# Performance work log

Measured on AMD Instinct MI355X. Metric: run time of the kernel, lower is better.

## Reference

```python
import jax, jax.numpy as jnp
import numpy as np

CUTOFF = 5.0       # module __init__ arg
BOX_L = 40.0       # side of cubic region positions are drawn from (OBC: no box passed)
N_ATOMS = 8192
MAX_PAIRS = 1_048_576  # static bound on directed pairs (expected ~550k)


def setup_inputs() -> dict:
    key = jax.random.key(0)
    positions = jax.random.uniform(key, (N_ATOMS, 3), dtype=jnp.float32) * BOX_L
    return {"positions": positions}


def _pairwise_dist(x):
    # Euclidean distance matrix via the gram trick (avoids [N,N,3] intermediate).
    sq = jnp.sum(x * x, axis=1)
    d2 = sq[:, None] + sq[None, :] - 2.0 * (x @ x.T)
    return jnp.sqrt(jnp.maximum(d2, 0.0))


def _safe_norm(dr):
    # norm with zero-safe gradient (padded pairs have dr == 0)
    d2 = jnp.sum(dr * dr, axis=1)
    ok = d2 > 0
    return jnp.where(ok, jnp.sqrt(jnp.where(ok, d2, 1.0)), 0.0)


def reference(positions):
    n = positions.shape[0]
    dist = _pairwise_dist(positions)                      # [N, N]
    mask = (dist < CUTOFF) & (~jnp.eye(n, dtype=bool))    # exclude self-pairs
    # torch.argwhere equivalent, padded to static size; padding -> (0, 0)
    i, j = jnp.nonzero(mask, size=MAX_PAIRS, fill_value=0)
    pairs = jnp.stack([i, j], axis=1).astype(jnp.int32)   # [MAX_PAIRS, 2]
    # pairs_buffer_scales: 1 where i < j else 0 (padding (0,0) -> 0)
    buffer_scales = (i < j).astype(jnp.int32)
    # pairs_ds (pbc_flag=False): ||r_j - r_i||
    dr = positions[j] - positions[i]                      # [MAX_PAIRS, 3]
    ds = _safe_norm(dr)
    return pairs, buffer_scales, ds
```

## Files before the change

### kernel.cpp

```cpp
#include <hip/hip_runtime.h>

#define MAXP 1048576
#define NATOMS 8192
#define D2_CUT 0x1.8ffffep+4f
#define CINV 0.175f
#define CAP 192

#define W_SORTPOS 0
#define W_SORTID  32768
#define W_ROWCNT  36864
#define W_GRPSUM  45056
#define W_CELLOFF 45568
#define W_JBUF    46080

__device__ __forceinline__ float sq3_nc(float x, float y, float z) {
#pragma clang fp contract(off)
  float a = x * x;
  float b = y * y;
  float c = z * z;
  return (a + b) + c;
}

__device__ __forceinline__ float d2_gram(float xi, float yi, float zi, float sqi,
                                         float xj, float yj, float zj, float sqj) {
#pragma clang fp contract(off)
  float g = xi * xj;
  g = __builtin_fmaf(yi, yj, g);
  g = __builtin_fmaf(zi, zj, g);
  float t = sqi + sqj;
  float d2 = t - 2.0f * g;
  return d2;
}

__device__ __forceinline__ float d2_direct(float xi, float yi, float zi,
                                           float xj, float yj, float zj) {
#pragma clang fp contract(off)
  float dx = xj - xi;
  float dy = yj - yi;
  float dz = zj - zi;
  float a = dx * dx;
  float b = dy * dy;
  float c = dz * dz;
  return (a + b) + c;
}

__device__ __forceinline__ int cellco(float v) {
  int c = (int)(v * CINV);
  return c < 0 ? 0 : (c > 6 ? 6 : c);
}

__global__ __launch_bounds__(256) void nl_pack(float* __restrict__ out,
                                               float* __restrict__ ws) {
  const int gtid = blockIdx.x * 256 + threadIdx.x;
  float4* o4 = (float4*)out;
#pragma unroll
  for (int k = 0; k < 16; ++k)
    o4[k * 65536 + gtid] = make_float4(0.f, 0.f, 0.f, 0.f);
  if (gtid < 512) ((int*)(ws + W_GRPSUM))[gtid] = 0;
}

__global__ __launch_bounds__(1024) void nl_prep(const float* __restrict__ pos,
                                                float* __restrict__ ws) {
  __shared__ int hcnt[343];
  __shared__ int hoff[344];
  __shared__ int hcur[343];
  __shared__ int s[512];
  const int tid = threadIdx.x;
  if (tid < 343) { hcnt[tid] = 0; hcur[tid] = 0; }
  __syncthreads();

  float x[8], y[8], z[8];
  int cl[8];
#pragma unroll
  for (int k = 0; k < 8; ++k) {
    int a = tid + k * 1024;
    x[k] = pos[3 * a]; y[k] = pos[3 * a + 1]; z[k] = pos[3 * a + 2];
    cl[k] = cellco(x[k]) + 7 * cellco(y[k]) + 49 * cellco(z[k]);
    atomicAdd(&hcnt[cl[k]], 1);
  }
  __syncthreads();

  if (tid < 512) s[tid] = (tid < 343) ? hcnt[tid] : 0;
  __syncthreads();
  for (int off = 1; off < 512; off <<= 1) {
    int v = (tid < 512 && tid >= off) ? s[tid - off] : 0;
    __syncthreads();
    if (tid < 512) s[tid] += v;
    __syncthreads();
  }
  if (tid < 343) hoff[tid] = (tid == 0) ? 0 : s[tid - 1];
  if (tid == 343) hoff[343] = NATOMS;
  __syncthreads();
  if (tid < 344) ((int*)(ws + W_CELLOFF))[tid] = hoff[tid];

  unsigned short* sortid = (unsigned short*)(ws + W_SORTID);
  float4* sortpos = (float4*)(ws + W_SORTPOS);
#pragma unroll
  for (int k = 0; k < 8; ++k) {
    int slot = hoff[cl[k]] + atomicAdd(&hcur[cl[k]], 1);
    sortid[slot] = (unsigned short)(tid + k * 1024);
    sortpos[slot] = make_float4(x[k], y[k], z[k], sq3_nc(x[k], y[k], z[k]));
  }
}

__global__ __launch_bounds__(256, 8) void nl_detect(float* __restrict__ ws) {
  __shared__ unsigned int bmap[4][256];
  __shared__ unsigned short stj[4][CAP];
  const int lane = threadIdx.x & 63;
  const int wave = threadIdx.x >> 6;
  const int slot = blockIdx.x * 4 + wave;

  const float4* __restrict__ sp4 = (const float4*)(ws + W_SORTPOS);
  const unsigned short* __restrict__ sid = (const unsigned short*)(ws + W_SORTID);
  const int* __restrict__ celloff = (const int*)(ws + W_CELLOFF);
  int* rowcnt = (int*)(ws + W_ROWCNT);
  int* grpsum = (int*)(ws + W_GRPSUM);
  unsigned short* jbuf = (unsigned short*)(ws + W_JBUF);

#pragma unroll
  for (int q = 0; q < 4; ++q) bmap[wave][lane + 64 * q] = 0u;

  const float4 pi = sp4[slot];
  const int rid = sid[slot];
  int cx = cellco(pi.x), cy = cellco(pi.y), cz = cellco(pi.z);
  int x0 = max(cx - 1, 0), x1 = min(cx + 1, 6);
  int y0 = max(cy - 1, 0), y1 = min(cy + 1, 6);
  int z0 = max(cz - 1, 0), z1 = min(cz + 1, 6);

  for (int icz = z0; icz <= z1; ++icz)
    for (int icy = y0; icy <= y1; ++icy) {
      int cb = 7 * icy + 49 * icz;
      int st = celloff[cb + x0];
      int en = celloff[cb + x1 + 1];
      for (int bb = st; bb < en; bb += 64) {
        int t = bb + lane;
        bool v = t < en;
        int t2 = v ? t : (en - 1);
        float4 p = sp4[t2];
        int jd = sid[t2];
        float d2 = d2_gram(pi.x, pi.y, pi.z, pi.w, p.x, p.y, p.z, p.w);
        if (v && d2 < D2_CUT)
          atomicOr(&bmap[wave][jd >> 5], 1u << (jd & 31));
      }
    }
  if (lane == 0)
    atomicAnd(&bmap[wave][rid >> 5], ~(1u << (rid & 31)));

  int ktot = 0;
#pragma unroll
  for (int seg = 0; seg < 4; ++seg) {
    int w = seg * 64 + lane;
    unsigned bits = bmap[wave][w];
    int pc = __popc(bits);
    int incl = pc;
    for (int d = 1; d < 64; d <<= 1) {
      int u = __shfl_up(incl, d, 64);
      if (lane >= d) incl += u;
    }
    int bpos = ktot + incl - pc;
    while (bits) {
      int b = __builtin_ctz(bits);
      bits &= bits - 1;
      if (bpos < CAP) stj[wave][bpos] = (unsigned short)(w * 32 + b);
      ++bpos;
    }
    ktot += __shfl(incl, 63, 64);
  }

  int k = ktot > CAP ? CAP : ktot;
  for (int s2 = lane; s2 < k; s2 += 64)
    jbuf[slot * CAP + s2] = stj[wave][s2];
  if (lane == 0) {
    rowcnt[rid] = ktot;
    atomicAdd(&grpsum[rid >> 6], ktot);
  }
}

__global__ __launch_bounds__(256, 8) void nl_emit(const float* __restrict__ pos,
                                                  float* __restrict__ out,
                                                  const float* __restrict__ ws) {
  const int lane = threadIdx.x & 63;
  const int wave = threadIdx.x >> 6;
  const int slot = blockIdx.x * 4 + wave;

  const float4* __restrict__ sp4 = (const float4*)(ws + W_SORTPOS);
  const unsigned short* __restrict__ sid = (const unsigned short*)(ws + W_SORTID);
  const int* __restrict__ rowcnt = (const int*)(ws + W_ROWCNT);
  const int* __restrict__ grpsum = (const int*)(ws + W_GRPSUM);
  const unsigned short* __restrict__ jbuf = (const unsigned short*)(ws + W_JBUF);

  const float4 pi = sp4[slot];
  const int rid = sid[slot];

  const int G = rid >> 6;
  int pre = ((lane < G) ? grpsum[lane] : 0) +
            ((lane + 64 < G) ? grpsum[lane + 64] : 0) +
            ((lane < (rid & 63)) ? rowcnt[(rid & ~63) + lane] : 0);
  for (int off = 32; off > 0; off >>= 1) pre += __shfl_down(pre, off, 64);
  const int ro = __shfl(pre, 0, 64);

  int k = rowcnt[rid];
  if (k > CAP) k = CAP;
  for (int s2 = lane; s2 < k; s2 += 64) {
    int j = jbuf[slot * CAP + s2];
    int o = ro + s2;
    if ((unsigned)o < MAXP) {
      float xj = pos[3 * j], yj = pos[3 * j + 1], zj = pos[3 * j + 2];
      float ds = sqrtf(d2_direct(pi.x, pi.y, pi.z, xj, yj, zj));
      ((float2*)out)[o] = make_float2((float)rid, (float)j);
      out[2 * MAXP + o] = (rid < j) ? 1.0f : 0.0f;
      out[3 * MAXP + o] = ds;
    }
  }
}

extern "C" void kernel_launch(void* const* d_in, const int* in_sizes, int n_in,
                              void* d_out, int out_size, void* d_ws, size_t ws_size,
                              hipStream_t stream) {
  const float* pos = (const float*)d_in[0];
  float* out = (float*)d_out;
  float* ws = (float*)d_ws;

  nl_pack<<<256, 256, 0, stream>>>(out, ws);
  nl_prep<<<1, 1024, 0, stream>>>(pos, ws);
  nl_detect<<<2048, 256, 0, stream>>>(ws);
  nl_emit<<<2048, 256, 0, stream>>>(pos, out, ws);
}
```

Measured before the change: 104.1 us.

## Fuse zeroing, detection and emission into one cooperative grid-synced kernel

```diff
diff --git a/kernel.cpp b/kernel.cpp
--- a/kernel.cpp
+++ b/kernel.cpp
@@ -1,4 +1,7 @@
 #include <hip/hip_runtime.h>
+#include <hip/hip_cooperative_groups.h>
+
+namespace cg = cooperative_groups;
 
 #define MAXP 1048576
 #define NATOMS 8192
@@ -49,16 +52,6 @@
   return c < 0 ? 0 : (c > 6 ? 6 : c);
 }
 
-__global__ __launch_bounds__(256) void nl_pack(float* __restrict__ out,
-                                               float* __restrict__ ws) {
-  const int gtid = blockIdx.x * 256 + threadIdx.x;
-  float4* o4 = (float4*)out;
-#pragma unroll
-  for (int k = 0; k < 16; ++k)
-    o4[k * 65536 + gtid] = make_float4(0.f, 0.f, 0.f, 0.f);
-  if (gtid < 512) ((int*)(ws + W_GRPSUM))[gtid] = 0;
-}
-
 __global__ __launch_bounds__(1024) void nl_prep(const float* __restrict__ pos,
                                                 float* __restrict__ ws) {
   __shared__ int hcnt[343];
@@ -67,6 +60,7 @@
   __shared__ int s[512];
   const int tid = threadIdx.x;
   if (tid < 343) { hcnt[tid] = 0; hcur[tid] = 0; }
+  if (tid < 512) ((int*)(ws + W_GRPSUM))[tid] = 0;
   __syncthreads();
 
   float x[8], y[8], z[8];
@@ -103,12 +97,20 @@
   }
 }
 
-__global__ __launch_bounds__(256, 8) void nl_detect(float* __restrict__ ws) {
+__global__ __launch_bounds__(256, 8) void nl_fused(const float* __restrict__ pos,
+                                                   float* __restrict__ out,
+                                                   float* __restrict__ ws,
+                                                   int coop) {
   __shared__ unsigned int bmap[4][256];
   __shared__ unsigned short stj[4][CAP];
-  const int lane = threadIdx.x & 63;
-  const int wave = threadIdx.x >> 6;
+  const int tid = threadIdx.x;
+  const int lane = tid & 63;
+  const int wave = tid >> 6;
   const int slot = blockIdx.x * 4 + wave;
+
+  float4* o4 = (float4*)out;
+  o4[blockIdx.x * 512 + tid] = make_float4(0.f, 0.f, 0.f, 0.f);
+  o4[blockIdx.x * 512 + 256 + tid] = make_float4(0.f, 0.f, 0.f, 0.f);
 
   const float4* __restrict__ sp4 = (const float4*)(ws + W_SORTPOS);
   const unsigned short* __restrict__ sid = (const unsigned short*)(ws + W_SORTID);
@@ -168,11 +170,34 @@
   }
 
   int k = ktot > CAP ? CAP : ktot;
-  for (int s2 = lane; s2 < k; s2 += 64)
-    jbuf[slot * CAP + s2] = stj[wave][s2];
+  if (!coop)
+    for (int s2 = lane; s2 < k; s2 += 64) jbuf[slot * CAP + s2] = stj[wave][s2];
   if (lane == 0) {
     rowcnt[rid] = ktot;
     atomicAdd(&grpsum[rid >> 6], ktot);
+  }
+
+  if (!coop) return;
+
+  cg::this_grid().sync();
+
+  const int G = rid >> 6;
+  int pre = ((lane < G) ? grpsum[lane] : 0) +
+            ((lane + 64 < G) ? grpsum[lane + 64] : 0) +
+            ((lane < (rid & 63)) ? rowcnt[(rid & ~63) + lane] : 0);
+  for (int off = 32; off > 0; off >>= 1) pre += __shfl_down(pre, off, 64);
+  const int ro = __shfl(pre, 0, 64);
+
+  for (int s2 = lane; s2 < k; s2 += 64) {
+    int j = stj[wave][s2];
+    int o = ro + s2;
+    if ((unsigned)o < MAXP) {
+      float xj = pos[3 * j], yj = pos[3 * j + 1], zj = pos[3 * j + 2];
+      float ds = sqrtf(d2_direct(pi.x, pi.y, pi.z, xj, yj, zj));
+      ((float2*)out)[o] = make_float2((float)rid, (float)j);
+      out[2 * MAXP + o] = (rid < j) ? 1.0f : 0.0f;
+      out[3 * MAXP + o] = ds;
+    }
   }
 }
 
@@ -221,8 +246,14 @@
   float* out = (float*)d_out;
   float* ws = (float*)d_ws;
 
-  nl_pack<<<256, 256, 0, stream>>>(out, ws);
   nl_prep<<<1, 1024, 0, stream>>>(pos, ws);
-  nl_detect<<<2048, 256, 0, stream>>>(ws);
-  nl_emit<<<2048, 256, 0, stream>>>(pos, out, ws);
-}
+
+  int coop = 1;
+  void* args[] = {(void*)&pos, (void*)&out, (void*)&ws, (void*)&coop};
+  hipError_t e = hipLaunchCooperativeKernel((const void*)nl_fused, dim3(2048),
+                                            dim3(256), args, 0, stream);
+  if (e != hipSuccess) {
+    nl_fused<<<2048, 256, 0, stream>>>(pos, out, ws, 0);
+    nl_emit<<<2048, 256, 0, stream>>>(pos, out, ws);
+  }
+}
```

Result: slower. 305.7 us (+193.6%).
